# Kernel tuning notes

Measured on AMD Instinct MI355X. Metric: run time of the kernel, lower is better.

The kernel has to match this reference:

```python
import jax, jax.numpy as jnp
import numpy as np

B, C, H, W = 32, 1024, 32, 32
KC, VC = 1024, 1024  # key_channels must equal H*W; value_channels must equal in_channels


def setup_inputs() -> dict:
    key = jax.random.key(0)
    ks = jax.random.split(key, 8)
    s = 1.0 / np.sqrt(C)
    return {
        "x": jax.random.normal(ks[0], (B, C, H, W), dtype=jnp.float32),
        "Wq": jax.random.normal(ks[1], (KC, C), dtype=jnp.float32) * s,
        "bq": jax.random.normal(ks[2], (KC,), dtype=jnp.float32) * 0.01,
        "Wk": jax.random.normal(ks[3], (KC, C), dtype=jnp.float32) * s,
        "bk": jax.random.normal(ks[4], (KC,), dtype=jnp.float32) * 0.01,
        "Wv": jax.random.normal(ks[5], (VC, C), dtype=jnp.float32) * s,
        "bv": jax.random.normal(ks[6], (VC,), dtype=jnp.float32) * 0.01,
        # torch init is zeros(1); use a nonzero scalar so the attention path is exercised
        "gamma": jax.random.normal(ks[7], (1,), dtype=jnp.float32) * 0.5,
    }


def reference(x, Wq, bq, Wk, bk, Wv, bv, gamma):
    b, c, h, w = x.shape
    n = h * w
    xf = x.reshape(b, c, n)  # [B, C, N]
    # 1x1 convs == per-position channel projections
    q = jnp.einsum('kc,bcn->bkn', Wq, xf) + bq[None, :, None]  # [B, Kc, N]
    k = jnp.einsum('kc,bcn->bkn', Wk, xf) + bk[None, :, None]  # [B, Kc, N]
    v = jnp.einsum('vc,bcn->bvn', Wv, xf) + bv[None, :, None]  # [B, Cv, N]
    # bmm(query, key^T): contracts spatial dim -> channel-channel attention [B, Kc, Kc]
    attn = jax.nn.softmax(jnp.einsum('bin,bjn->bij', q, k), axis=-1)
    # bmm(value, attention): value's spatial dim (== Kc) contracts with attn rows
    out = jnp.einsum('bvn,bnk->bvk', v, attn)  # [B, Cv, Kc] with Kc == N
    out = out.reshape(b, -1, h, w)
    return gamma * out + x
```

## Files before the change

### kernel.cpp

```cpp
#include <hip/hip_runtime.h>
#include <cstdint>

typedef __fp16 f16x8 __attribute__((ext_vector_type(8)));
typedef __fp16 f16x4 __attribute__((ext_vector_type(4)));
typedef float  f32x4 __attribute__((ext_vector_type(4)));

static constexpr int NDIM = 1024;

static constexpr long long OFF_W     = 0;
static constexpr long long OFF_BIAS  = 6291456;
static constexpr long long OFF_XT    = 6303744;
static constexpr long long OFF_S     = 0;
static constexpr long long OFF_QKV   = 134217728;
static constexpr long long OFF_STATS = OFF_QKV + 2097152;

__device__ __forceinline__ void async16(__fp16* lds, const __fp16* g) {
  __builtin_amdgcn_global_load_lds(
      (const __attribute__((address_space(1))) void*)g,
      (__attribute__((address_space(3))) void*)lds, 16, 0, 0);
}

__global__ __launch_bounds__(256) void cast_w(const float* __restrict__ Wq,
                                              const float* __restrict__ Wk,
                                              const float* __restrict__ Wv,
                                              __fp16* __restrict__ W3) {
  const int i = blockIdx.x * 256 + threadIdx.x;
  const int which = i >> 18;
  const int j = i & 262143;
  const float* src = which == 0 ? Wq : (which == 1 ? Wk : Wv);
  const float4 v = ((const float4*)src)[j];
  f16x4 o = {(__fp16)v.x, (__fp16)v.y, (__fp16)v.z, (__fp16)v.w};
  ((f16x4*)W3)[i] = o;
}

__global__ __launch_bounds__(256) void pack_bias(const float* __restrict__ bq,
                                                 const float* __restrict__ bk,
                                                 const float* __restrict__ bv,
                                                 float* __restrict__ b3) {
  const int i = blockIdx.x * 256 + threadIdx.x;
  if (i < 1024) b3[i] = bq[i];
  else if (i < 2048) b3[i] = bk[i - 1024];
  else if (i < 3072) b3[i] = bv[i - 2048];
}

__global__ __launch_bounds__(256) void transpose_cast_x(const float* __restrict__ x,
                                                        __fp16* __restrict__ xT) {
  __shared__ float t[32][33];
  const int b = blockIdx.z;
  const int n0 = blockIdx.x * 32, c0 = blockIdx.y * 32;
  const float* xb = x + (long long)b * NDIM * NDIM;
  __fp16* ob = xT + (long long)b * NDIM * NDIM;
  const int tx = threadIdx.x & 31, ty = threadIdx.x >> 5;
#pragma unroll
  for (int i = ty; i < 32; i += 8)
    t[i][tx] = xb[(long long)(c0 + i) * NDIM + n0 + tx];
  __syncthreads();
#pragma unroll
  for (int i = ty; i < 32; i += 8)
    ob[(long long)(n0 + i) * NDIM + c0 + tx] = (__fp16)t[tx][i];
}


#define STAGE_A(NXT, KN)                                                            \
  async16(&As[(NXT)*8192 + tid*8],        A  + (long long)(m0 + sRow)       * 1024 + (KN) + sCol); \
  async16(&As[(NXT)*8192 + 4096 + tid*8], A  + (long long)(m0 + 128 + sRow) * 1024 + (KN) + sCol);

#define STAGE_B(NXT, KN)                                                            \
  async16(&Bs[(NXT)*8192 + tid*8],        Bp + (long long)(n0 + sRow)       * 1024 + (KN) + sCol); \
  async16(&Bs[(NXT)*8192 + 4096 + tid*8], Bp + (long long)(n0 + 128 + sRow) * 1024 + (KN) + sCol);

#define TILE(BUF, NXT, KN)                                                          \
  asm volatile("s_waitcnt vmcnt(8)" ::: "memory");                                  \
  __builtin_amdgcn_s_barrier();                                                     \
  STAGE_A(NXT, KN)                                                                  \
  STAGE_B(NXT, KN)                                                                  \
  bf[0] = *(const f16x8*)&Bs[(BUF)*8192 + bBase + 0*512];                           \
  bf[1] = *(const f16x8*)&Bs[(BUF)*8192 + bBase + 1*512];                           \
  _Pragma("unroll")                                                                 \
  for (int mf = 0; mf < 8; ++mf)                                                    \
    af[mf] = *(const f16x8*)&As[(BUF)*8192 + aBase + mf*512];                       \
  bf[2] = *(const f16x8*)&Bs[(BUF)*8192 + bBase + 2*512];                           \
  bf[3] = *(const f16x8*)&Bs[(BUF)*8192 + bBase + 3*512];                           \
  _Pragma("unroll")                                                                 \
  for (int mf = 0; mf < 8; ++mf) {                                                  \
    _Pragma("unroll")                                                               \
    for (int nf = 0; nf < 4; ++nf)                                                  \
      acc[mf][nf] = __builtin_amdgcn_mfma_f32_16x16x32_f16(af[mf], bf[nf], acc[mf][nf], 0, 0, 0); \
  }

template <int EPI>
__global__ __launch_bounds__(512, 2)
void gemm256(const __fp16* __restrict__ Ag, const __fp16* __restrict__ Bg,
             void* __restrict__ Cout, const float* __restrict__ bias,
             const float* __restrict__ X, const float* __restrict__ gamma,
             long long sA, long long sB, long long sC) {
  __shared__ alignas(16) __fp16 As[4 * 8192];
  __shared__ alignas(16) __fp16 Bs[4 * 8192];

  const int tid  = threadIdx.x;
  const int wid  = tid >> 6, lane = tid & 63;
  const int wm   = wid >> 2, wn = wid & 3;
  const int g    = lane >> 4, r = lane & 15;
  const int b    = blockIdx.z;
  const int m0   = blockIdx.y * 256;
  const int n0   = blockIdx.x * 256;

  const __fp16* A  = Ag + (long long)b * sA;
  const __fp16* Bp = Bg + (long long)b * sB;

  const int sRow = tid >> 2;
  const int sCol = ((tid & 3) ^ ((tid >> 3) & 3)) * 8;

  const int fcol  = (g ^ ((r >> 1) & 3)) * 8;
  const int aBase = (wm * 128 + r) * 32 + fcol;
  const int bBase = (wn * 64 + r) * 32 + fcol;

  f16x8 af[8];
  f16x8 bf[4];
  f32x4 acc[8][4];
#pragma unroll
  for (int i = 0; i < 8; ++i)
#pragma unroll
    for (int j = 0; j < 4; ++j) acc[i][j] = f32x4{0.f, 0.f, 0.f, 0.f};

  STAGE_A(0, 0)  STAGE_B(0, 0)
  STAGE_A(1, 32) STAGE_B(1, 32)
  STAGE_A(2, 64) STAGE_B(2, 64)

  for (int t0 = 0; t0 < 1024; t0 += 128) {
    const int ka  = t0 + 96;
    const int k0n = (ka < 1024) ? ka : 0;
    const int k1n = (ka + 32 < 1024) ? ka + 32 : 0;
    const int k2n = (ka + 64 < 1024) ? ka + 64 : 0;
    const int k3n = (ka + 96 < 1024) ? ka + 96 : 0;
    TILE(0, 3, k0n)
    TILE(1, 0, k1n)
    TILE(2, 1, k2n)
    TILE(3, 2, k3n)
  }

  const float g2 = (EPI == 2) ? gamma[0] : 0.f;
  const int ccol  = n0 + wn * 64 + (lane & 15);
  const int crow0 = m0 + wm * 128 + (lane >> 4) * 4;
#pragma unroll
  for (int mf = 0; mf < 8; ++mf) {
#pragma unroll
    for (int reg = 0; reg < 4; ++reg) {
      const int row = crow0 + mf * 16 + reg;
      const long long rb = (long long)b * sC + (long long)row * 1024;
      const float bb = (EPI == 0) ? bias[row] : 0.f;
#pragma unroll
      for (int nf = 0; nf < 4; ++nf) {
        const int col = ccol + nf * 16;
        const float v = acc[mf][nf][reg];
        if (EPI == 0)      ((__fp16*)Cout)[rb + col] = (__fp16)(v + bb);
        else if (EPI == 1) ((float*)Cout)[rb + col] = v;
        else               ((float*)Cout)[rb + col] = g2 * v + X[rb + col];
      }
    }
  }
}

__global__ __launch_bounds__(256) void row_stats(const float* __restrict__ S,
                                                 float2* __restrict__ stats) {
  const int row = blockIdx.x * 4 + (threadIdx.x >> 6);
  const int lane = threadIdx.x & 63;
  const float4* rp = (const float4*)(S + (long long)row * NDIM);
  float4 v[4];
  float m = -3.4e38f;
#pragma unroll
  for (int j = 0; j < 4; j++) {
    v[j] = rp[lane + 64 * j];
    m = fmaxf(m, fmaxf(fmaxf(v[j].x, v[j].y), fmaxf(v[j].z, v[j].w)));
  }
#pragma unroll
  for (int o = 32; o; o >>= 1) m = fmaxf(m, __shfl_xor(m, o));
  float s = 0.f;
#pragma unroll
  for (int j = 0; j < 4; j++)
    s += __expf(v[j].x - m) + __expf(v[j].y - m) + __expf(v[j].z - m) + __expf(v[j].w - m);
#pragma unroll
  for (int o = 32; o; o >>= 1) s += __shfl_xor(s, o);
  if (lane == 0) stats[row] = make_float2(m, 1.f / s);
}

__global__ __launch_bounds__(256) void softmax_transpose(const float* __restrict__ S,
                                                         const float2* __restrict__ stats,
                                                         __fp16* __restrict__ attnT) {
  __shared__ __fp16 t[64][72];
  const int b = blockIdx.z;
  const int i0 = blockIdx.y * 64, j0 = blockIdx.x * 64;
  const float* Sb = S + (long long)b * NDIM * NDIM;
  const float2* st = stats + b * NDIM;
  const int tr = threadIdx.x >> 4;
  const int tc = (threadIdx.x & 15) * 4;
#pragma unroll
  for (int it = 0; it < 4; it++) {
    const int i = tr + 16 * it;
    const float4 vv = *(const float4*)&Sb[(long long)(i0 + i) * NDIM + j0 + tc];
    const float2 ms = st[i0 + i];
    t[tc + 0][i] = (__fp16)(__expf(vv.x - ms.x) * ms.y);
    t[tc + 1][i] = (__fp16)(__expf(vv.y - ms.x) * ms.y);
    t[tc + 2][i] = (__fp16)(__expf(vv.z - ms.x) * ms.y);
    t[tc + 3][i] = (__fp16)(__expf(vv.w - ms.x) * ms.y);
  }
  __syncthreads();
  __fp16* Ab = attnT + (long long)b * 3145728;
#pragma unroll
  for (int it = 0; it < 4; it++) {
    const int j = tr + 16 * it;
    f16x4 o = {t[j][tc], t[j][tc + 1], t[j][tc + 2], t[j][tc + 3]};
    *(f16x4*)&Ab[(long long)(j0 + j) * NDIM + i0 + tc] = o;
  }
}

extern "C" void kernel_launch(void* const* d_in, const int* in_sizes, int n_in,
                              void* d_out, int out_size, void* d_ws, size_t ws_size,
                              hipStream_t stream) {
  const float* x     = (const float*)d_in[0];
  const float* Wq    = (const float*)d_in[1];
  const float* bq    = (const float*)d_in[2];
  const float* Wk    = (const float*)d_in[3];
  const float* bk    = (const float*)d_in[4];
  const float* Wv    = (const float*)d_in[5];
  const float* bv    = (const float*)d_in[6];
  const float* gamma = (const float*)d_in[7];
  char* ws = (char*)d_ws;

  __fp16* W3    = (__fp16*)(ws + OFF_W);
  float*  bias3 = (float*)(ws + OFF_BIAS);
  __fp16* xT    = (__fp16*)(ws + OFF_XT);
  float*  S     = (float*)(ws + OFF_S);
  __fp16* QKV   = (__fp16*)(ws + OFF_QKV);
  float2* stats = (float2*)(ws + OFF_STATS);
  float*  out   = (float*)d_out;

  cast_w<<<3072, 256, 0, stream>>>(Wq, Wk, Wv, W3);
  pack_bias<<<12, 256, 0, stream>>>(bq, bk, bv, bias3);
  transpose_cast_x<<<dim3(32, 32, 32), 256, 0, stream>>>(x, xT);

  gemm256<0><<<dim3(4, 12, 32), 512, 0, stream>>>(
      W3, xT, QKV, bias3, nullptr, nullptr,
      0LL, 1048576LL, 3145728LL);

  gemm256<1><<<dim3(4, 4, 32), 512, 0, stream>>>(
      QKV, QKV + 1048576, S, nullptr, nullptr, nullptr,
      3145728LL, 3145728LL, 1048576LL);

  row_stats<<<8192, 256, 0, stream>>>(S, stats);
  softmax_transpose<<<dim3(16, 16, 32), 256, 0, stream>>>(S, stats, QKV);

  gemm256<2><<<dim3(4, 4, 32), 512, 0, stream>>>(
      QKV + 2097152, QKV, out, nullptr, x, gamma,
      3145728LL, 3145728LL, 1048576LL);
}
```

Before: 529.4 us.

## Restructure GEMM main loop into double-buffered K=64 phases with XCD-aware grid swizzle

Replaces the 4-stage K=32 ring with a 2-stage K=64 double buffer whose staging of the next tile is interleaved with four MFMA phases per tile, using setprio and sched_barrier around each phase. Wave layout changes from 2x4 to 4x2, so each wave computes a 64x128 sub-tile, and the LDS swizzle is widened to 8 columns. The 3D grid is flattened into a 1D grid with a modulo-8 block swizzle that remaps tiles across XCDs for better L2 locality. Per-wave vmcnt waits are staggered by wave class. The intent is better overlap of global-to-LDS loads with MFMA work, at the cost of more barriers and more complex synchronization.

```diff
diff --git a/kernel.cpp b/kernel.cpp
--- a/kernel.cpp
+++ b/kernel.cpp
@@ -61,32 +61,74 @@
 }
 
 
-#define STAGE_A(NXT, KN)                                                            \
-  async16(&As[(NXT)*8192 + tid*8],        A  + (long long)(m0 + sRow)       * 1024 + (KN) + sCol); \
-  async16(&As[(NXT)*8192 + 4096 + tid*8], A  + (long long)(m0 + 128 + sRow) * 1024 + (KN) + sCol);
-
-#define STAGE_B(NXT, KN)                                                            \
-  async16(&Bs[(NXT)*8192 + tid*8],        Bp + (long long)(n0 + sRow)       * 1024 + (KN) + sCol); \
-  async16(&Bs[(NXT)*8192 + 4096 + tid*8], Bp + (long long)(n0 + 128 + sRow) * 1024 + (KN) + sCol);
-
-#define TILE(BUF, NXT, KN)                                                          \
-  asm volatile("s_waitcnt vmcnt(8)" ::: "memory");                                  \
-  __builtin_amdgcn_s_barrier();                                                     \
-  STAGE_A(NXT, KN)                                                                  \
-  STAGE_B(NXT, KN)                                                                  \
-  bf[0] = *(const f16x8*)&Bs[(BUF)*8192 + bBase + 0*512];                           \
-  bf[1] = *(const f16x8*)&Bs[(BUF)*8192 + bBase + 1*512];                           \
-  _Pragma("unroll")                                                                 \
-  for (int mf = 0; mf < 8; ++mf)                                                    \
-    af[mf] = *(const f16x8*)&As[(BUF)*8192 + aBase + mf*512];                       \
-  bf[2] = *(const f16x8*)&Bs[(BUF)*8192 + bBase + 2*512];                           \
-  bf[3] = *(const f16x8*)&Bs[(BUF)*8192 + bBase + 3*512];                           \
-  _Pragma("unroll")                                                                 \
-  for (int mf = 0; mf < 8; ++mf) {                                                  \
-    _Pragma("unroll")                                                               \
-    for (int nf = 0; nf < 4; ++nf)                                                  \
-      acc[mf][nf] = __builtin_amdgcn_mfma_f32_16x16x32_f16(af[mf], bf[nf], acc[mf][nf], 0, 0, 0); \
-  }
+#define LDA(c, mf, ks) \
+  (*(const f16x8*)&As[(c)*16384 + aRowBase + (mf)*1024 + ((ks) ? ac1 : ac0)])
+#define LDB_(c, nf, ks) \
+  (*(const f16x8*)&Bs[(c)*16384 + bRowBase + (nf)*1024 + ((ks) ? ac1 : ac0)])
+
+#define STAGE_AH(dst, h, kk)                                                          \
+  async16(&As[(dst)*16384 + (h)*8192 + tid*8],                                        \
+          A + (long long)(m0 + (h)*128 + sRow) * 1024 + (kk) + sCol);                 \
+  async16(&As[(dst)*16384 + (h)*8192 + 4096 + tid*8],                                 \
+          A + (long long)(m0 + (h)*128 + 64 + sRow) * 1024 + (kk) + sCol);
+
+#define STAGE_BH(dst, h, kk)                                                          \
+  async16(&Bs[(dst)*16384 + (h)*8192 + tid*8],                                        \
+          Bp + (long long)(n0 + (h)*128 + sRow) * 1024 + (kk) + sCol);                \
+  async16(&Bs[(dst)*16384 + (h)*8192 + 4096 + tid*8],                                 \
+          Bp + (long long)(n0 + (h)*128 + 64 + sRow) * 1024 + (kk) + sCol);
+
+#define MFMA_PH(nfp)                                                                  \
+  asm volatile("s_waitcnt lgkmcnt(0)" ::: "memory");                                  \
+  __builtin_amdgcn_sched_barrier(0);                                                  \
+  __builtin_amdgcn_s_setprio(1);                                                      \
+  _Pragma("unroll")                                                                   \
+  for (int mq = 0; mq < 4; ++mq) {                                                    \
+    acc[mq][(nfp)]     = __builtin_amdgcn_mfma_f32_16x16x32_f16(af[mq][0], bf[0][0], acc[mq][(nfp)],     0, 0, 0); \
+    acc[mq][(nfp)]     = __builtin_amdgcn_mfma_f32_16x16x32_f16(af[mq][1], bf[0][1], acc[mq][(nfp)],     0, 0, 0); \
+    acc[mq][(nfp) + 1] = __builtin_amdgcn_mfma_f32_16x16x32_f16(af[mq][0], bf[1][0], acc[mq][(nfp) + 1], 0, 0, 0); \
+    acc[mq][(nfp) + 1] = __builtin_amdgcn_mfma_f32_16x16x32_f16(af[mq][1], bf[1][1], acc[mq][(nfp) + 1], 0, 0, 0); \
+  }                                                                                   \
+  __builtin_amdgcn_s_setprio(0);                                                      \
+  __builtin_amdgcn_sched_barrier(0);
+
+#define WAIT_CLASS                                                                    \
+  if (cls == 0)      asm volatile("s_waitcnt vmcnt(4)" ::: "memory");                 \
+  else if (cls == 1) asm volatile("s_waitcnt vmcnt(2)" ::: "memory");                 \
+  else               asm volatile("s_waitcnt vmcnt(0)" ::: "memory");
+
+#define TILE(c, knext)                                                                \
+                                                                              \
+  _Pragma("unroll")                                                                   \
+  for (int mq = 0; mq < 4; ++mq) { af[mq][0] = LDA(c, mq, 0); af[mq][1] = LDA(c, mq, 1); } \
+  bf[0][0] = LDB_(c, 0, 0); bf[0][1] = LDB_(c, 0, 1);                                 \
+  bf[1][0] = LDB_(c, 1, 0); bf[1][1] = LDB_(c, 1, 1);                                 \
+  STAGE_AH((c) ^ 1, 0, knext)                                                         \
+  STAGE_BH((c) ^ 1, 0, knext)                                                         \
+  __builtin_amdgcn_s_barrier();                                                       \
+  MFMA_PH(0)                                                                          \
+  __builtin_amdgcn_s_barrier();                                                       \
+                                                                              \
+  bf[0][0] = LDB_(c, 2, 0); bf[0][1] = LDB_(c, 2, 1);                                 \
+  bf[1][0] = LDB_(c, 3, 0); bf[1][1] = LDB_(c, 3, 1);                                 \
+  STAGE_AH((c) ^ 1, 1, knext)                                                         \
+  STAGE_BH((c) ^ 1, 1, knext)                                                         \
+  __builtin_amdgcn_s_barrier();                                                       \
+  MFMA_PH(2)                                                                          \
+  __builtin_amdgcn_s_barrier();                                                       \
+                                                                              \
+  bf[0][0] = LDB_(c, 4, 0); bf[0][1] = LDB_(c, 4, 1);                                 \
+  bf[1][0] = LDB_(c, 5, 0); bf[1][1] = LDB_(c, 5, 1);                                 \
+  __builtin_amdgcn_s_barrier();                                                       \
+  MFMA_PH(4)                                                                          \
+  __builtin_amdgcn_s_barrier();                                                       \
+                                                                              \
+  bf[0][0] = LDB_(c, 6, 0); bf[0][1] = LDB_(c, 6, 1);                                 \
+  bf[1][0] = LDB_(c, 7, 0); bf[1][1] = LDB_(c, 7, 1);                                 \
+  __builtin_amdgcn_s_barrier();                                                       \
+  MFMA_PH(6)                                                                          \
+  WAIT_CLASS                                                                          \
+  __builtin_amdgcn_s_barrier();
 
 template <int EPI>
 __global__ __launch_bounds__(512, 2)
@@ -94,63 +136,68 @@
              void* __restrict__ Cout, const float* __restrict__ bias,
              const float* __restrict__ X, const float* __restrict__ gamma,
              long long sA, long long sB, long long sC) {
-  __shared__ alignas(16) __fp16 As[4 * 8192];
-  __shared__ alignas(16) __fp16 Bs[4 * 8192];
+  __shared__ alignas(16) __fp16 As[2 * 16384];
+  __shared__ alignas(16) __fp16 Bs[2 * 16384];
 
   const int tid  = threadIdx.x;
   const int wid  = tid >> 6, lane = tid & 63;
-  const int wm   = wid >> 2, wn = wid & 3;
+  const int wm   = wid >> 1, wn = wid & 1;
   const int g    = lane >> 4, r = lane & 15;
-  const int b    = blockIdx.z;
-  const int m0   = blockIdx.y * 256;
-  const int n0   = blockIdx.x * 256;
+
+  const int nwg = gridDim.x;
+  const int bid = blockIdx.x;
+  const int swz = (bid & 7) * (nwg >> 3) + (bid >> 3);
+  const int bx = swz & 3, bz = (swz >> 2) & 31, by = swz >> 7;
+  const int b = bz, m0 = by * 256, n0 = bx * 256;
 
   const __fp16* A  = Ag + (long long)b * sA;
   const __fp16* Bp = Bg + (long long)b * sB;
 
-  const int sRow = tid >> 2;
-  const int sCol = ((tid & 3) ^ ((tid >> 3) & 3)) * 8;
-
-  const int fcol  = (g ^ ((r >> 1) & 3)) * 8;
-  const int aBase = (wm * 128 + r) * 32 + fcol;
-  const int bBase = (wn * 64 + r) * 32 + fcol;
-
-  f16x8 af[8];
-  f16x8 bf[4];
-  f32x4 acc[8][4];
-#pragma unroll
-  for (int i = 0; i < 8; ++i)
-#pragma unroll
-    for (int j = 0; j < 4; ++j) acc[i][j] = f32x4{0.f, 0.f, 0.f, 0.f};
-
-  STAGE_A(0, 0)  STAGE_B(0, 0)
-  STAGE_A(1, 32) STAGE_B(1, 32)
-  STAGE_A(2, 64) STAGE_B(2, 64)
-
-  for (int t0 = 0; t0 < 1024; t0 += 128) {
-    const int ka  = t0 + 96;
-    const int k0n = (ka < 1024) ? ka : 0;
-    const int k1n = (ka + 32 < 1024) ? ka + 32 : 0;
-    const int k2n = (ka + 64 < 1024) ? ka + 64 : 0;
-    const int k3n = (ka + 96 < 1024) ? ka + 96 : 0;
-    TILE(0, 3, k0n)
-    TILE(1, 0, k1n)
-    TILE(2, 1, k2n)
-    TILE(3, 2, k3n)
+  const int sRow = tid >> 3;
+  const int sCol = ((tid & 7) ^ ((tid >> 3) & 7)) * 8;
+
+  const int ac0 = ((g) ^ (r & 7)) * 8;
+  const int ac1 = ((4 + g) ^ (r & 7)) * 8;
+  const int aRowBase = (wm * 64 + r) * 64;
+  const int bRowBase = (wn * 128 + r) * 64;
+
+  const int cls = (wn == 1) ? 2 : (wm >> 1);
+
+  f16x8 af[4][2];
+  f16x8 bf[2][2];
+  f32x4 acc[4][8];
+#pragma unroll
+  for (int i = 0; i < 4; ++i)
+#pragma unroll
+    for (int j = 0; j < 8; ++j) acc[i][j] = f32x4{0.f, 0.f, 0.f, 0.f};
+
+  STAGE_AH(0, 0, 0)
+  STAGE_BH(0, 0, 0)
+  STAGE_AH(0, 1, 0)
+  STAGE_BH(0, 1, 0)
+  WAIT_CLASS
+  __builtin_amdgcn_s_barrier();
+
+  for (int i = 0; i < 8; ++i) {
+    const int k0  = i * 128;
+    const int kn1 = k0 + 64;
+    const int kn2 = (k0 + 128 < 1024) ? k0 + 128 : 0;
+    TILE(0, kn1)
+    TILE(1, kn2)
   }
 
   const float g2 = (EPI == 2) ? gamma[0] : 0.f;
-  const int ccol  = n0 + wn * 64 + (lane & 15);
-  const int crow0 = m0 + wm * 128 + (lane >> 4) * 4;
-#pragma unroll
-  for (int mf = 0; mf < 8; ++mf) {
+  const int ccol  = n0 + wn * 128 + (lane & 15);
+  const int crow0 = m0 + wm * 64 + (lane >> 4) * 4;
+#pragma unroll
+  for (int mf = 0; mf < 4; ++mf) {
 #pragma unroll
     for (int reg = 0; reg < 4; ++reg) {
       const int row = crow0 + mf * 16 + reg;
       const long long rb = (long long)b * sC + (long long)row * 1024;
       const float bb = (EPI == 0) ? bias[row] : 0.f;
 #pragma unroll
-      for (int nf = 0; nf < 4; ++nf) {
+      for (int nf = 0; nf < 8; ++nf) {
         const int col = ccol + nf * 16;
         const float v = acc[mf][nf][reg];
         if (EPI == 0)      ((__fp16*)Cout)[rb + col] = (__fp16)(v + bb);
@@ -239,18 +286,18 @@
   pack_bias<<<12, 256, 0, stream>>>(bq, bk, bv, bias3);
   transpose_cast_x<<<dim3(32, 32, 32), 256, 0, stream>>>(x, xT);
 
-  gemm256<0><<<dim3(4, 12, 32), 512, 0, stream>>>(
+  gemm256<0><<<1536, 512, 0, stream>>>(
       W3, xT, QKV, bias3, nullptr, nullptr,
       0LL, 1048576LL, 3145728LL);
 
-  gemm256<1><<<dim3(4, 4, 32), 512, 0, stream>>>(
+  gemm256<1><<<512, 512, 0, stream>>>(
       QKV, QKV + 1048576, S, nullptr, nullptr, nullptr,
       3145728LL, 3145728LL, 1048576LL);
 
   row_stats<<<8192, 256, 0, stream>>>(S, stats);
   softmax_transpose<<<dim3(16, 16, 32), 256, 0, stream>>>(S, stats, QKV);
 
-  gemm256<2><<<dim3(4, 4, 32), 512, 0, stream>>>(
+  gemm256<2><<<512, 512, 0, stream>>>(
       QKV + 2097152, QKV, out, nullptr, x, gamma,
       3145728LL, 3145728LL, 1048576LL);
 }
```

Result: slower. 585.4 us (+10.6%).

## Shrink GEMM tile to 256x128 with 3-stage pipeline and higher occupancy

Applied to the files above, without the earlier changes.

Changes the GEMM block tile from 256x256 to 256x128. Each of the 8 waves now computes a 64x64 sub-tile instead of 128x64, so accumulator registers drop by half. The LDS ring goes from 4 stages to 3 stages, and launch bounds now ask for 4 blocks per CU. The grids double in x to match. The aim is to raise occupancy and hide latency better. The cost is less data reuse per block and more global traffic.

```diff
diff --git a/kernel.cpp b/kernel.cpp
--- a/kernel.cpp
+++ b/kernel.cpp
@@ -61,49 +61,38 @@
 }
 
 
-#define STAGE_A(NXT, KN)                                                            \
-  async16(&As[(NXT)*8192 + tid*8],        A  + (long long)(m0 + sRow)       * 1024 + (KN) + sCol); \
-  async16(&As[(NXT)*8192 + 4096 + tid*8], A  + (long long)(m0 + 128 + sRow) * 1024 + (KN) + sCol);
-
-#define STAGE_B(NXT, KN)                                                            \
-  async16(&Bs[(NXT)*8192 + tid*8],        Bp + (long long)(n0 + sRow)       * 1024 + (KN) + sCol); \
-  async16(&Bs[(NXT)*8192 + 4096 + tid*8], Bp + (long long)(n0 + 128 + sRow) * 1024 + (KN) + sCol);
-
-#define TILE(BUF, NXT, KN)                                                          \
-  asm volatile("s_waitcnt vmcnt(8)" ::: "memory");                                  \
-  __builtin_amdgcn_s_barrier();                                                     \
-  STAGE_A(NXT, KN)                                                                  \
-  STAGE_B(NXT, KN)                                                                  \
-  bf[0] = *(const f16x8*)&Bs[(BUF)*8192 + bBase + 0*512];                           \
-  bf[1] = *(const f16x8*)&Bs[(BUF)*8192 + bBase + 1*512];                           \
-  _Pragma("unroll")                                                                 \
-  for (int mf = 0; mf < 8; ++mf)                                                    \
-    af[mf] = *(const f16x8*)&As[(BUF)*8192 + aBase + mf*512];                       \
-  bf[2] = *(const f16x8*)&Bs[(BUF)*8192 + bBase + 2*512];                           \
-  bf[3] = *(const f16x8*)&Bs[(BUF)*8192 + bBase + 3*512];                           \
-  _Pragma("unroll")                                                                 \
-  for (int mf = 0; mf < 8; ++mf) {                                                  \
-    _Pragma("unroll")                                                               \
-    for (int nf = 0; nf < 4; ++nf)                                                  \
-      acc[mf][nf] = __builtin_amdgcn_mfma_f32_16x16x32_f16(af[mf], bf[nf], acc[mf][nf], 0, 0, 0); \
-  }
+#define TILE(CA, CB, NA, NB, KN)                                                   \
+  asm volatile("s_waitcnt vmcnt(3)" ::: "memory");                                 \
+  __builtin_amdgcn_s_barrier();                                                    \
+  async16(&As[(NA) + tid*8],        A  + (long long)(m0 + sRow)       * 1024 + (KN) + sCol); \
+  async16(&As[(NA) + 4096 + tid*8], A  + (long long)(m0 + 128 + sRow) * 1024 + (KN) + sCol); \
+  async16(&Bs[(NB) + tid*8],        Bp + (long long)(n0 + sRow)       * 1024 + (KN) + sCol); \
+  _Pragma("unroll")                                                                \
+  for (int mf = 0; mf < 4; ++mf) af[mf] = *(const f16x8*)&As[(CA) + aBase + mf*512]; \
+  _Pragma("unroll")                                                                \
+  for (int nf = 0; nf < 4; ++nf) bf[nf] = *(const f16x8*)&Bs[(CB) + bBase + nf*512]; \
+  _Pragma("unroll")                                                                \
+  for (int mf = 0; mf < 4; ++mf)                                                   \
+    _Pragma("unroll")                                                              \
+    for (int nf = 0; nf < 4; ++nf)                                                 \
+      acc[mf][nf] = __builtin_amdgcn_mfma_f32_16x16x32_f16(af[mf], bf[nf], acc[mf][nf], 0, 0, 0);
 
 template <int EPI>
-__global__ __launch_bounds__(512, 2)
+__global__ __launch_bounds__(512, 4)
 void gemm256(const __fp16* __restrict__ Ag, const __fp16* __restrict__ Bg,
              void* __restrict__ Cout, const float* __restrict__ bias,
              const float* __restrict__ X, const float* __restrict__ gamma,
              long long sA, long long sB, long long sC) {
-  __shared__ alignas(16) __fp16 As[4 * 8192];
-  __shared__ alignas(16) __fp16 Bs[4 * 8192];
+  __shared__ alignas(16) __fp16 As[3 * 8192];
+  __shared__ alignas(16) __fp16 Bs[3 * 4096];
 
   const int tid  = threadIdx.x;
   const int wid  = tid >> 6, lane = tid & 63;
-  const int wm   = wid >> 2, wn = wid & 3;
+  const int wm   = wid >> 1, wn = wid & 1;
   const int g    = lane >> 4, r = lane & 15;
   const int b    = blockIdx.z;
   const int m0   = blockIdx.y * 256;
-  const int n0   = blockIdx.x * 256;
+  const int n0   = blockIdx.x * 128;
 
   const __fp16* A  = Ag + (long long)b * sA;
   const __fp16* Bp = Bg + (long long)b * sB;
@@ -112,38 +101,37 @@
   const int sCol = ((tid & 3) ^ ((tid >> 3) & 3)) * 8;
 
   const int fcol  = (g ^ ((r >> 1) & 3)) * 8;
-  const int aBase = (wm * 128 + r) * 32 + fcol;
+  const int aBase = (wm * 64 + r) * 32 + fcol;
   const int bBase = (wn * 64 + r) * 32 + fcol;
 
-  f16x8 af[8];
+  f16x8 af[4];
   f16x8 bf[4];
-  f32x4 acc[8][4];
-#pragma unroll
-  for (int i = 0; i < 8; ++i)
+  f32x4 acc[4][4];
+#pragma unroll
+  for (int i = 0; i < 4; ++i)
 #pragma unroll
     for (int j = 0; j < 4; ++j) acc[i][j] = f32x4{0.f, 0.f, 0.f, 0.f};
 
-  STAGE_A(0, 0)  STAGE_B(0, 0)
-  STAGE_A(1, 32) STAGE_B(1, 32)
-  STAGE_A(2, 64) STAGE_B(2, 64)
-
-  for (int t0 = 0; t0 < 1024; t0 += 128) {
-    const int ka  = t0 + 96;
-    const int k0n = (ka < 1024) ? ka : 0;
-    const int k1n = (ka + 32 < 1024) ? ka + 32 : 0;
-    const int k2n = (ka + 64 < 1024) ? ka + 64 : 0;
-    const int k3n = (ka + 96 < 1024) ? ka + 96 : 0;
-    TILE(0, 3, k0n)
-    TILE(1, 0, k1n)
-    TILE(2, 1, k2n)
-    TILE(3, 2, k3n)
-  }
+  async16(&As[tid*8],               A  + (long long)(m0 + sRow)       * 1024 + sCol);
+  async16(&As[4096 + tid*8],        A  + (long long)(m0 + 128 + sRow) * 1024 + sCol);
+  async16(&Bs[tid*8],               Bp + (long long)(n0 + sRow)       * 1024 + sCol);
+  async16(&As[8192 + tid*8],        A  + (long long)(m0 + sRow)       * 1024 + 32 + sCol);
+  async16(&As[8192 + 4096 + tid*8], A  + (long long)(m0 + 128 + sRow) * 1024 + 32 + sCol);
+  async16(&Bs[4096 + tid*8],        Bp + (long long)(n0 + sRow)       * 1024 + 32 + sCol);
+
+  for (int k0 = 0; k0 < 960; k0 += 96) {
+    TILE(0,     0,    16384, 8192, k0 + 64)
+    TILE(8192,  4096, 0,     0,    k0 + 96)
+    TILE(16384, 8192, 8192,  4096, k0 + 128)
+  }
+  TILE(0,     0,    16384, 8192, 0)
+  TILE(8192,  4096, 0,     0,    0)
 
   const float g2 = (EPI == 2) ? gamma[0] : 0.f;
-  const int ccol  = n0 + wn * 64 + (lane & 15);
-  const int crow0 = m0 + wm * 128 + (lane >> 4) * 4;
-#pragma unroll
-  for (int mf = 0; mf < 8; ++mf) {
+  const int ccol  = n0 + wn * 64 + r;
+  const int crow0 = m0 + wm * 64 + g * 4;
+#pragma unroll
+  for (int mf = 0; mf < 4; ++mf) {
 #pragma unroll
     for (int reg = 0; reg < 4; ++reg) {
       const int row = crow0 + mf * 16 + reg;
@@ -239,18 +227,18 @@
   pack_bias<<<12, 256, 0, stream>>>(bq, bk, bv, bias3);
   transpose_cast_x<<<dim3(32, 32, 32), 256, 0, stream>>>(x, xT);
 
-  gemm256<0><<<dim3(4, 12, 32), 512, 0, stream>>>(
+  gemm256<0><<<dim3(8, 12, 32), 512, 0, stream>>>(
       W3, xT, QKV, bias3, nullptr, nullptr,
       0LL, 1048576LL, 3145728LL);
 
-  gemm256<1><<<dim3(4, 4, 32), 512, 0, stream>>>(
+  gemm256<1><<<dim3(8, 4, 32), 512, 0, stream>>>(
       QKV, QKV + 1048576, S, nullptr, nullptr, nullptr,
       3145728LL, 3145728LL, 1048576LL);
 
   row_stats<<<8192, 256, 0, stream>>>(S, stats);
   softmax_transpose<<<dim3(16, 16, 32), 256, 0, stream>>>(S, stats, QKV);
 
-  gemm256<2><<<dim3(4, 4, 32), 512, 0, stream>>>(
+  gemm256<2><<<dim3(8, 4, 32), 512, 0, stream>>>(
       QKV + 2097152, QKV, out, nullptr, x, gamma,
       3145728LL, 3145728LL, 1048576LL);
 }
```

After: 612.4 us. 15.7% more time.

## Software-pipeline LDS fragment reads across k-tiles in the fp16 MFMA GEMM

Applied to the files above, without the earlier changes.

The GEMM main loop is restructured so the first half of the next tile's A/B fragments is read from LDS while the current tile's MFMAs run. Fragments are split into ping-pong register sets, and the global-load wait is relaxed from vmcnt(8) to vmcnt(4). The MFMA groups are fenced with lgkmcnt waits, sched_barrier and s_setprio so LDS latency overlaps with matrix math. This adds register pressure and tighter scheduling constraints under the existing two-blocks-per-CU launch bound.

```diff
diff --git a/kernel.cpp b/kernel.cpp
--- a/kernel.cpp
+++ b/kernel.cpp
@@ -61,32 +61,66 @@
 }
 
 
-#define STAGE_A(NXT, KN)                                                            \
-  async16(&As[(NXT)*8192 + tid*8],        A  + (long long)(m0 + sRow)       * 1024 + (KN) + sCol); \
-  async16(&As[(NXT)*8192 + 4096 + tid*8], A  + (long long)(m0 + 128 + sRow) * 1024 + (KN) + sCol);
-
-#define STAGE_B(NXT, KN)                                                            \
-  async16(&Bs[(NXT)*8192 + tid*8],        Bp + (long long)(n0 + sRow)       * 1024 + (KN) + sCol); \
-  async16(&Bs[(NXT)*8192 + 4096 + tid*8], Bp + (long long)(n0 + 128 + sRow) * 1024 + (KN) + sCol);
-
-#define TILE(BUF, NXT, KN)                                                          \
-  asm volatile("s_waitcnt vmcnt(8)" ::: "memory");                                  \
-  __builtin_amdgcn_s_barrier();                                                     \
-  STAGE_A(NXT, KN)                                                                  \
-  STAGE_B(NXT, KN)                                                                  \
-  bf[0] = *(const f16x8*)&Bs[(BUF)*8192 + bBase + 0*512];                           \
-  bf[1] = *(const f16x8*)&Bs[(BUF)*8192 + bBase + 1*512];                           \
-  _Pragma("unroll")                                                                 \
-  for (int mf = 0; mf < 8; ++mf)                                                    \
-    af[mf] = *(const f16x8*)&As[(BUF)*8192 + aBase + mf*512];                       \
-  bf[2] = *(const f16x8*)&Bs[(BUF)*8192 + bBase + 2*512];                           \
-  bf[3] = *(const f16x8*)&Bs[(BUF)*8192 + bBase + 3*512];                           \
-  _Pragma("unroll")                                                                 \
-  for (int mf = 0; mf < 8; ++mf) {                                                  \
-    _Pragma("unroll")                                                               \
-    for (int nf = 0; nf < 4; ++nf)                                                  \
-      acc[mf][nf] = __builtin_amdgcn_mfma_f32_16x16x32_f16(af[mf], bf[nf], acc[mf][nf], 0, 0, 0); \
-  }
+#define STAGE4(NXT, KN)                                                                  \
+  async16(&As[(NXT) + tid*8],        A  + (long long)(m0 + sRow)       * 1024 + (KN) + sCol); \
+  async16(&As[(NXT) + 4096 + tid*8], A  + (long long)(m0 + 128 + sRow) * 1024 + (KN) + sCol); \
+  async16(&Bs[(NXT) + tid*8],        Bp + (long long)(n0 + sRow)       * 1024 + (KN) + sCol); \
+  async16(&Bs[(NXT) + 4096 + tid*8], Bp + (long long)(n0 + 128 + sRow) * 1024 + (KN) + sCol);
+
+#define READ_A(S, BUF)                                  \
+  S##a[0] = *(const f16x8*)&As[(BUF) + aBase + 0*512];  \
+  S##a[1] = *(const f16x8*)&As[(BUF) + aBase + 1*512];  \
+  S##a[2] = *(const f16x8*)&As[(BUF) + aBase + 2*512];  \
+  S##a[3] = *(const f16x8*)&As[(BUF) + aBase + 3*512];  \
+  S##b[0] = *(const f16x8*)&Bs[(BUF) + bBase + 0*512];  \
+  S##b[1] = *(const f16x8*)&Bs[(BUF) + bBase + 1*512];
+
+#define READ_L(BUF)                                     \
+  la[0] = *(const f16x8*)&As[(BUF) + aBase + 4*512];    \
+  la[1] = *(const f16x8*)&As[(BUF) + aBase + 5*512];    \
+  la[2] = *(const f16x8*)&As[(BUF) + aBase + 6*512];    \
+  la[3] = *(const f16x8*)&As[(BUF) + aBase + 7*512];    \
+  lb[0] = *(const f16x8*)&Bs[(BUF) + bBase + 2*512];    \
+  lb[1] = *(const f16x8*)&Bs[(BUF) + bBase + 3*512];
+
+#define MFMA_G1(S)                                                                         \
+  _Pragma("unroll")                                                                        \
+  for (int mf = 0; mf < 4; ++mf) {                                                         \
+    acc[mf][0] = __builtin_amdgcn_mfma_f32_16x16x32_f16(S##a[mf], S##b[0], acc[mf][0], 0, 0, 0); \
+    acc[mf][1] = __builtin_amdgcn_mfma_f32_16x16x32_f16(S##a[mf], S##b[1], acc[mf][1], 0, 0, 0); \
+  }
+
+#define MFMA_REST(S)                                                                       \
+  _Pragma("unroll")                                                                        \
+  for (int mf = 0; mf < 4; ++mf) {                                                         \
+    acc[mf][2] = __builtin_amdgcn_mfma_f32_16x16x32_f16(S##a[mf], lb[0], acc[mf][2], 0, 0, 0);   \
+    acc[mf][3] = __builtin_amdgcn_mfma_f32_16x16x32_f16(S##a[mf], lb[1], acc[mf][3], 0, 0, 0);   \
+  }                                                                                        \
+  _Pragma("unroll")                                                                        \
+  for (int mf = 0; mf < 4; ++mf) {                                                         \
+    acc[4+mf][0] = __builtin_amdgcn_mfma_f32_16x16x32_f16(la[mf], S##b[0], acc[4+mf][0], 0, 0, 0); \
+    acc[4+mf][1] = __builtin_amdgcn_mfma_f32_16x16x32_f16(la[mf], S##b[1], acc[4+mf][1], 0, 0, 0); \
+    acc[4+mf][2] = __builtin_amdgcn_mfma_f32_16x16x32_f16(la[mf], lb[0],   acc[4+mf][2], 0, 0, 0); \
+    acc[4+mf][3] = __builtin_amdgcn_mfma_f32_16x16x32_f16(la[mf], lb[1],   acc[4+mf][3], 0, 0, 0); \
+  }
+
+#define TILE(BUF, NBUF, NXT, KN, CUR, NX)                        \
+  asm volatile("s_waitcnt vmcnt(4)" ::: "memory");               \
+  __builtin_amdgcn_s_barrier();                                  \
+  STAGE4(NXT, KN)                                                \
+  READ_L(BUF)                                                    \
+  READ_A(NX, NBUF)                                               \
+  asm volatile("s_waitcnt lgkmcnt(12)" ::: "memory");            \
+  __builtin_amdgcn_sched_barrier(0);                             \
+  __builtin_amdgcn_s_setprio(1);                                 \
+  MFMA_G1(CUR)                                                   \
+  __builtin_amdgcn_s_setprio(0);                                 \
+  asm volatile("s_waitcnt lgkmcnt(6)" ::: "memory");             \
+  __builtin_amdgcn_sched_barrier(0);                             \
+  __builtin_amdgcn_s_setprio(1);                                 \
+  MFMA_REST(CUR)                                                 \
+  __builtin_amdgcn_s_setprio(0);                                 \
+  __builtin_amdgcn_sched_barrier(0);
 
 template <int EPI>
 __global__ __launch_bounds__(512, 2)
@@ -115,33 +149,35 @@
   const int aBase = (wm * 128 + r) * 32 + fcol;
   const int bBase = (wn * 64 + r) * 32 + fcol;
 
-  f16x8 af[8];
-  f16x8 bf[4];
+  f16x8 Pa[4], Pb[2], Qa[4], Qb[2], la[4], lb[2];
   f32x4 acc[8][4];
 #pragma unroll
   for (int i = 0; i < 8; ++i)
 #pragma unroll
     for (int j = 0; j < 4; ++j) acc[i][j] = f32x4{0.f, 0.f, 0.f, 0.f};
 
-  STAGE_A(0, 0)  STAGE_B(0, 0)
-  STAGE_A(1, 32) STAGE_B(1, 32)
-  STAGE_A(2, 64) STAGE_B(2, 64)
-
-  for (int t0 = 0; t0 < 1024; t0 += 128) {
-    const int ka  = t0 + 96;
+  STAGE4(0, 0)
+  STAGE4(8192, 32)
+  STAGE4(16384, 64)
+  asm volatile("s_waitcnt vmcnt(4)" ::: "memory");
+  __builtin_amdgcn_s_barrier();
+  READ_A(P, 0)
+
+  for (int k0 = 0; k0 < 1024; k0 += 128) {
+    const int ka  = k0 + 96;
     const int k0n = (ka < 1024) ? ka : 0;
     const int k1n = (ka + 32 < 1024) ? ka + 32 : 0;
     const int k2n = (ka + 64 < 1024) ? ka + 64 : 0;
     const int k3n = (ka + 96 < 1024) ? ka + 96 : 0;
-    TILE(0, 3, k0n)
-    TILE(1, 0, k1n)
-    TILE(2, 1, k2n)
-    TILE(3, 2, k3n)
+    TILE(0,     8192,  24576, k0n, P, Q)
+    TILE(8192,  16384, 0,     k1n, Q, P)
+    TILE(16384, 24576, 8192,  k2n, P, Q)
+    TILE(24576, 0,     16384, k3n, Q, P)
   }
 
   const float g2 = (EPI == 2) ? gamma[0] : 0.f;
-  const int ccol  = n0 + wn * 64 + (lane & 15);
-  const int crow0 = m0 + wm * 128 + (lane >> 4) * 4;
+  const int ccol  = n0 + wn * 64 + r;
+  const int crow0 = m0 + wm * 128 + g * 4;
 #pragma unroll
   for (int mf = 0; mf < 8; ++mf) {
 #pragma unroll
```

After: 568.0 us. 7.3% more time.
